# Optimization experiments

Hardware: AMD Instinct MI355X
Metric: run time of the kernel (lower is better)

The kernel has to match this reference:

```python
import jax, jax.numpy as jnp
import numpy as np

PH, PW = 7, 7
SPATIAL_SCALE = 0.0625


def _hat_int(t):
    # Antiderivative of the unit hat (triangle) function phi(t)=max(0,1-|t|),
    # i.e. integral_{-inf}^{t} phi. Piecewise quadratic, saturates to [0,1].
    t = jnp.clip(t, -1.0, 1.0)
    return jnp.where(t <= 0, 0.5 * (t + 1.0) ** 2, 1.0 - 0.5 * (1.0 - t) ** 2)


def _bin_weights(lo, hi, size):
    # lo, hi: [R, P] continuous bin boundaries (in feature-map coordinates).
    # Returns [R, P, size]: exact 1D integral of the hat basis at each integer
    # grid node over [lo, hi]. Bilinear interpolation is the tensor product of
    # 1D hat bases, so the exact 2D PrRoI integral separates into these weights.
    grid = jnp.arange(size, dtype=lo.dtype)
    return _hat_int(hi[..., None] - grid) - _hat_int(lo[..., None] - grid)


def _prroi_pool(features, rois):
    N, C, H, W = features.shape
    R = rois.shape[0]
    dt = features.dtype
    bidx = rois[:, 0].astype(jnp.int32)
    x1 = rois[:, 1] * SPATIAL_SCALE
    y1 = rois[:, 2] * SPATIAL_SCALE
    x2 = rois[:, 3] * SPATIAL_SCALE
    y2 = rois[:, 4] * SPATIAL_SCALE
    roi_w = jnp.maximum(x2 - x1, 0.0)
    roi_h = jnp.maximum(y2 - y1, 0.0)
    bw = roi_w / PW  # [R]
    bh = roi_h / PH
    px = jnp.arange(PW, dtype=dt)
    py = jnp.arange(PH, dtype=dt)
    x_lo = x1[:, None] + px[None, :] * bw[:, None]  # [R, PW]
    x_hi = x_lo + bw[:, None]
    y_lo = y1[:, None] + py[None, :] * bh[:, None]  # [R, PH]
    y_hi = y_lo + bh[:, None]
    Wx = _bin_weights(x_lo, x_hi, W)  # [R, PW, W]
    Wy = _bin_weights(y_lo, y_hi, H)  # [R, PH, H]
    area = bw * bh  # [R]
    inv_area = jnp.where(area > 0, 1.0 / jnp.maximum(area, 1e-12), 0.0)
    out = jnp.zeros((R, C, PH, PW), dtype=dt)
    for n in range(N):  # small fixed batch loop; avoids [R,C,H,W] gather
        m = (bidx == n).astype(dt)
        out = out + jnp.einsum('rph,chw,rqw->rcpq', Wy * m[:, None, None], features[n], Wx)
    return out * inv_area[:, None, None, None]


def setup_inputs() -> dict:
    key = jax.random.key(0)
    k1, k2, k3, k4, k5, k6 = jax.random.split(key, 6)
    N, C, H, W, R = 2, 256, 152, 152, 512
    features = jax.random.normal(k1, (N, C, H, W), dtype=jnp.float32)
    img = H / SPATIAL_SCALE  # 2432 px image
    bidx = jax.random.randint(k2, (R,), 0, N).astype(jnp.float32)
    x1 = jax.random.uniform(k3, (R,), minval=0.0, maxval=img * 0.7)
    y1 = jax.random.uniform(k4, (R,), minval=0.0, maxval=img * 0.7)
    x2 = x1 + jax.random.uniform(k5, (R,), minval=32.0, maxval=img * 0.3)
    y2 = y1 + jax.random.uniform(k6, (R,), minval=32.0, maxval=img * 0.3)
    rois = jnp.stack([bidx, x1, y1, x2, y2], axis=1).astype(jnp.float32)
    return {"features": features, "rois": rois}


def reference(features, rois):
    return _prroi_pool(features, rois)
```

## Files before the change

### kernel.cpp

```cpp
#include <hip/hip_runtime.h>

#define PHH 7
#define PWW 7
static constexpr float SPATIAL_SCALE = 0.0625f;

__device__ __forceinline__ float hat_int(float t) {
    t = fminf(fmaxf(t, -1.0f), 1.0f);
    float a = t + 1.0f, b = 1.0f - t;
    return (t <= 0.0f) ? 0.5f * a * a : 1.0f - 0.5f * b * b;
}

__device__ __forceinline__ float bin_w(float lo, float hi, float g) {
    return hat_int(hi - g) - hat_int(lo - g);
}

__device__ __forceinline__ unsigned short f32_to_bf16_rne(float x) {
    unsigned int u = __float_as_uint(x);
    unsigned int r = 0x7FFFu + ((u >> 16) & 1u);
    return (unsigned short)((u + r) >> 16);
}

__device__ __forceinline__ float bf_lo(unsigned int v) {
    return __uint_as_float(v << 16);
}
__device__ __forceinline__ float bf_hi(unsigned int v) {
    return __uint_as_float(v & 0xFFFF0000u);
}

__global__ __launch_bounds__(256) void transpose_nchw_nhwc_bf16(
    const float* __restrict__ src, unsigned short* __restrict__ dst, int C, int HW)
{
    __shared__ float tile[32][33];
    const int n = blockIdx.z;
    const int hw0 = blockIdx.x * 32;
    const int c0 = blockIdx.y * 32;
    const float* s = src + (size_t)n * C * HW;
    unsigned short* d = dst + (size_t)n * C * HW;
    const int tx = threadIdx.x, ty = threadIdx.y;
    #pragma unroll
    for (int i = ty; i < 32; i += 8) {
        int c = c0 + i, hw = hw0 + tx;
        if (c < C && hw < HW) tile[i][tx] = s[(size_t)c * HW + hw];
    }
    __syncthreads();
    #pragma unroll
    for (int i = ty; i < 32; i += 8) {
        int hw = hw0 + i, c = c0 + tx;
        if (c < C && hw < HW) d[(size_t)hw * C + c] = f32_to_bf16_rne(tile[tx][i]);
    }
}

__global__ __launch_bounds__(256) void prroi_pool_cs2(
    const unsigned short* __restrict__ ft,
    const float* __restrict__ rois,
    float* __restrict__ out,
    int H, int W, int R)
{
    const int nwg = R * PHH;
    int task = (int)blockIdx.x;
    if ((nwg & 7) == 0) {
        const int cpx = nwg >> 3;
        task = (task & 7) * cpx + (task >> 3);
    }
    const int r = task / PHH;
    const int p = task % PHH;

    const int tid = threadIdx.x;
    const int wig = tid >> 6;
    const int lane = tid & 63;
    const int chHalf = wig & 1;
    const int colWave = wig >> 1;
    const int c0 = chHalf * 128 + lane * 2;

    const float* roi = rois + (size_t)r * 5;
    const int b = (int)roi[0];
    const float x1 = roi[1] * SPATIAL_SCALE;
    const float y1 = roi[2] * SPATIAL_SCALE;
    const float x2 = roi[3] * SPATIAL_SCALE;
    const float y2 = roi[4] * SPATIAL_SCALE;
    const float bw = fmaxf(x2 - x1, 0.0f) / (float)PWW;
    const float bh = fmaxf(y2 - y1, 0.0f) / (float)PHH;
    const float area = bw * bh;
    const float inv_area = (area > 0.0f) ? 1.0f / fmaxf(area, 1e-12f) : 0.0f;

    const float ylo = y1 + (float)p * bh;
    const float yhi = ylo + bh;
    const int h0 = max(0, (int)ceilf(ylo - 1.0f));
    const int h1 = min(H - 1, (int)floorf(yhi + 1.0f));
    const int w0 = max(0, (int)ceilf(x1 - 1.0f));
    const int w1 = min(W - 1, (int)floorf(x2 + 1.0f));
    const int nh = min(h1 - h0 + 1, 16);
    const int ww = w1 - w0 + 1;
    const int wwpad = (ww + 7) & ~7;

    __shared__ float wx8[152 * 8];
    __shared__ float wys[16];
    __shared__ float rbuf[2 * 64 * 15];

    for (int i = tid; i < wwpad; i += 256) {
        const float g = (float)(w0 + i);
        #pragma unroll
        for (int q = 0; q < PWW; ++q) {
            const float lo = x1 + (float)q * bw;
            wx8[i * 8 + q] = (i < ww) ? bin_w(lo, lo + bw, g) * inv_area : 0.0f;
        }
        wx8[i * 8 + 7] = 0.0f;
    }
    for (int i = tid; i < nh; i += 256)
        wys[i] = bin_w(ylo, yhi, (float)(h0 + i));
    __syncthreads();

    float acc[PWW][2];
    #pragma unroll
    for (int q = 0; q < PWW; ++q) {
        acc[q][0] = 0.0f;
        acc[q][1] = 0.0f;
    }

    const size_t rowstride = (size_t)W * 256;
    const unsigned short* base =
        ft + ((size_t)b * H + (size_t)h0) * rowstride + (size_t)w0 * 256 + c0;

    for (int chunk = colWave * 8; chunk < ww; chunk += 16) {
        int off[8];
        #pragma unroll
        for (int j = 0; j < 8; ++j)
            off[j] = (chunk + j < ww) ? (chunk + j) * 256 : 0;

        float u[2][8];
        #pragma unroll
        for (int j = 0; j < 8; ++j) { u[0][j] = 0.0f; u[1][j] = 0.0f; }

        auto load_row = [&](unsigned int (&v)[8], int i) {
            const unsigned short* rp = base + (size_t)i * rowstride;
            #pragma unroll
            for (int j = 0; j < 8; ++j)
                v[j] = *(const unsigned int*)(rp + off[j]);
        };
        auto fma_row = [&](const unsigned int (&v)[8], float wy) {
            #pragma unroll
            for (int j = 0; j < 8; ++j) {
                u[0][j] = fmaf(wy, bf_lo(v[j]), u[0][j]);
                u[1][j] = fmaf(wy, bf_hi(v[j]), u[1][j]);
            }
        };

        unsigned int A[8], B[8];
        load_row(A, 0);
        int i = 0;
        while (true) {
            if (i + 1 < nh) load_row(B, i + 1);
            fma_row(A, wys[i]);
            if (++i >= nh) break;
            if (i + 1 < nh) load_row(A, i + 1);
            fma_row(B, wys[i]);
            if (++i >= nh) break;
        }

        #pragma unroll
        for (int j = 0; j < 8; ++j) {
            const float4 wa = *(const float4*)&wx8[(chunk + j) * 8];
            const float4 wb = *(const float4*)&wx8[(chunk + j) * 8 + 4];
            acc[0][0] = fmaf(wa.x, u[0][j], acc[0][0]);
            acc[0][1] = fmaf(wa.x, u[1][j], acc[0][1]);
            acc[1][0] = fmaf(wa.y, u[0][j], acc[1][0]);
            acc[1][1] = fmaf(wa.y, u[1][j], acc[1][1]);
            acc[2][0] = fmaf(wa.z, u[0][j], acc[2][0]);
            acc[2][1] = fmaf(wa.z, u[1][j], acc[2][1]);
            acc[3][0] = fmaf(wa.w, u[0][j], acc[3][0]);
            acc[3][1] = fmaf(wa.w, u[1][j], acc[3][1]);
            acc[4][0] = fmaf(wb.x, u[0][j], acc[4][0]);
            acc[4][1] = fmaf(wb.x, u[1][j], acc[4][1]);
            acc[5][0] = fmaf(wb.y, u[0][j], acc[5][0]);
            acc[5][1] = fmaf(wb.y, u[1][j], acc[5][1]);
            acc[6][0] = fmaf(wb.z, u[0][j], acc[6][0]);
            acc[6][1] = fmaf(wb.z, u[1][j], acc[6][1]);
        }
    }

    float* pbuf = rbuf + chHalf * (64 * 15) + lane * 15;
    if (colWave == 1) {
        #pragma unroll
        for (int q = 0; q < PWW; ++q) {
            pbuf[q * 2 + 0] = acc[q][0];
            pbuf[q * 2 + 1] = acc[q][1];
        }
    }
    __syncthreads();
    if (colWave == 0) {
        float* o = out + ((size_t)r * 256 + c0) * (PHH * PWW) + p * PWW;
        #pragma unroll
        for (int q = 0; q < PWW; ++q) {
            o[q]             = acc[q][0] + pbuf[q * 2 + 0];
            o[PHH * PWW + q] = acc[q][1] + pbuf[q * 2 + 1];
        }
    }
}

__global__ __launch_bounds__(256) void prroi_pool_nchw(
    const float* __restrict__ f, const float* __restrict__ rois,
    float* __restrict__ out, int C, int H, int W, int R)
{
    const int idx = blockIdx.x * blockDim.x + threadIdx.x;
    const int total = R * C * PHH * PWW;
    if (idx >= total) return;
    const int q = idx % PWW;
    const int p = (idx / PWW) % PHH;
    const int c = (idx / (PWW * PHH)) % C;
    const int r = idx / (PWW * PHH * C);
    const float* roi = rois + (size_t)r * 5;
    const int b = (int)roi[0];
    const float x1 = roi[1] * SPATIAL_SCALE;
    const float y1 = roi[2] * SPATIAL_SCALE;
    const float x2 = roi[3] * SPATIAL_SCALE;
    const float y2 = roi[4] * SPATIAL_SCALE;
    const float bw = fmaxf(x2 - x1, 0.0f) / (float)PWW;
    const float bh = fmaxf(y2 - y1, 0.0f) / (float)PHH;
    const float area = bw * bh;
    const float inv_area = (area > 0.0f) ? 1.0f / fmaxf(area, 1e-12f) : 0.0f;
    const float xlo = x1 + (float)q * bw, xhi = xlo + bw;
    const float ylo = y1 + (float)p * bh, yhi = ylo + bh;
    const int h0 = max(0, (int)ceilf(ylo - 1.0f));
    const int h1 = min(H - 1, (int)floorf(yhi + 1.0f));
    const int w0 = max(0, (int)ceilf(xlo - 1.0f));
    const int w1 = min(W - 1, (int)floorf(xhi + 1.0f));
    float acc = 0.0f;
    for (int h = h0; h <= h1; ++h) {
        const float wy = bin_w(ylo, yhi, (float)h);
        const float* fr = f + (((size_t)b * C + c) * H + h) * W;
        for (int w = w0; w <= w1; ++w)
            acc = fmaf(wy * bin_w(xlo, xhi, (float)w), fr[w], acc);
    }
    out[idx] = acc * inv_area;
}

extern "C" void kernel_launch(void* const* d_in, const int* in_sizes, int n_in,
                              void* d_out, int out_size, void* d_ws, size_t ws_size,
                              hipStream_t stream)
{
    const float* features = (const float*)d_in[0];
    const float* rois = (const float*)d_in[1];
    float* out = (float*)d_out;

    const int C = 256, H = 152, W = 152;
    const int N = in_sizes[0] / (C * H * W);
    const int R = in_sizes[1] / 5;

    const size_t need = (size_t)N * C * H * W * sizeof(unsigned short);
    if (ws_size >= need && C == 256) {
        unsigned short* ft = (unsigned short*)d_ws;
        const int HW = H * W;
        dim3 tgrid((HW + 31) / 32, (C + 31) / 32, N);
        transpose_nchw_nhwc_bf16<<<tgrid, dim3(32, 8), 0, stream>>>(features, ft, C, HW);
        prroi_pool_cs2<<<R * PHH, 256, 0, stream>>>(ft, rois, out, H, W, R);
    } else {
        const int total = R * C * PHH * PWW;
        prroi_pool_nchw<<<(total + 255) / 256, 256, 0, stream>>>(features, rois, out, C, H, W, R);
    }
}
```

Measured before the change: 59.01 us.

## Use persistent atomic work-queue pooling kernel and wider bf16 transpose tiles

The pooling kernel becomes persistent: 2048 blocks repeatedly pull (roi, row) tasks from a global atomic counter instead of one block per task. The counter is reset by the transpose kernel that runs first. The transpose now uses 64x64 tiles, converts to bf16 before staging in shared memory, and writes two channels packed into each 32-bit store. The aim is to balance uneven per-task work and cut transpose store traffic. In exchange it drops the XCD-aware task swizzle, adds an atomic and an extra barrier per task, and reserves a fixed workspace offset for the counter.

Result: slower. 94.91 us (+60.9%).

```diff
diff --git a/kernel.cpp b/kernel.cpp
--- a/kernel.cpp
+++ b/kernel.cpp
@@ -27,44 +27,53 @@
     return __uint_as_float(v & 0xFFFF0000u);
 }
 
-__global__ __launch_bounds__(256) void transpose_nchw_nhwc_bf16(
-    const float* __restrict__ src, unsigned short* __restrict__ dst, int C, int HW)
-{
-    __shared__ float tile[32][33];
+__global__ __launch_bounds__(256) void transpose_nchw_nhwc_bf16_v2(
+    const float* __restrict__ src, unsigned short* __restrict__ dst,
+    int C, int HW, int* __restrict__ counter)
+{
+    if (blockIdx.x == 0 && blockIdx.y == 0 && blockIdx.z == 0 && threadIdx.x == 0)
+        *counter = 0;
+
+    __shared__ unsigned short tile[64][66];
     const int n = blockIdx.z;
-    const int hw0 = blockIdx.x * 32;
-    const int c0 = blockIdx.y * 32;
+    const int hw0 = blockIdx.x * 64;
+    const int c0 = blockIdx.y * 64;
     const float* s = src + (size_t)n * C * HW;
     unsigned short* d = dst + (size_t)n * C * HW;
-    const int tx = threadIdx.x, ty = threadIdx.y;
+
+    const int tx = threadIdx.x & 63;
+    const int ty = threadIdx.x >> 6;
     #pragma unroll
-    for (int i = ty; i < 32; i += 8) {
-        int c = c0 + i, hw = hw0 + tx;
-        if (c < C && hw < HW) tile[i][tx] = s[(size_t)c * HW + hw];
+    for (int i = 0; i < 16; ++i) {
+        const int cl = ty * 16 + i;
+        const int c = c0 + cl, hw = hw0 + tx;
+        if (c < C && hw < HW)
+            tile[cl][tx] = f32_to_bf16_rne(s[(size_t)c * HW + hw]);
     }
     __syncthreads();
+
+    const int cl = threadIdx.x & 31;
+    const int hb = threadIdx.x >> 5;
     #pragma unroll
-    for (int i = ty; i < 32; i += 8) {
-        int hw = hw0 + i, c = c0 + tx;
-        if (c < C && hw < HW) d[(size_t)hw * C + c] = f32_to_bf16_rne(tile[tx][i]);
-    }
-}
-
-__global__ __launch_bounds__(256) void prroi_pool_cs2(
+    for (int i = 0; i < 8; ++i) {
+        const int hwl = hb * 8 + i;
+        const int hw = hw0 + hwl;
+        const int c = c0 + 2 * cl;
+        if (hw < HW && c < C) {
+            const unsigned int v = (unsigned int)tile[2 * cl][hwl]
+                                 | ((unsigned int)tile[2 * cl + 1][hwl] << 16);
+            *(unsigned int*)(d + (size_t)hw * C + c) = v;
+        }
+    }
+}
+
+__global__ __launch_bounds__(256) void prroi_pool_persist(
     const unsigned short* __restrict__ ft,
     const float* __restrict__ rois,
     float* __restrict__ out,
-    int H, int W, int R)
-{
-    const int nwg = R * PHH;
-    int task = (int)blockIdx.x;
-    if ((nwg & 7) == 0) {
-        const int cpx = nwg >> 3;
-        task = (task & 7) * cpx + (task >> 3);
-    }
-    const int r = task / PHH;
-    const int p = task % PHH;
-
+    int H, int W, int R, int* __restrict__ counter)
+{
+    const int ntask = R * PHH;
     const int tid = threadIdx.x;
     const int wig = tid >> 6;
     const int lane = tid & 63;
@@ -72,127 +81,134 @@
     const int colWave = wig >> 1;
     const int c0 = chHalf * 128 + lane * 2;
 
-    const float* roi = rois + (size_t)r * 5;
-    const int b = (int)roi[0];
-    const float x1 = roi[1] * SPATIAL_SCALE;
-    const float y1 = roi[2] * SPATIAL_SCALE;
-    const float x2 = roi[3] * SPATIAL_SCALE;
-    const float y2 = roi[4] * SPATIAL_SCALE;
-    const float bw = fmaxf(x2 - x1, 0.0f) / (float)PWW;
-    const float bh = fmaxf(y2 - y1, 0.0f) / (float)PHH;
-    const float area = bw * bh;
-    const float inv_area = (area > 0.0f) ? 1.0f / fmaxf(area, 1e-12f) : 0.0f;
-
-    const float ylo = y1 + (float)p * bh;
-    const float yhi = ylo + bh;
-    const int h0 = max(0, (int)ceilf(ylo - 1.0f));
-    const int h1 = min(H - 1, (int)floorf(yhi + 1.0f));
-    const int w0 = max(0, (int)ceilf(x1 - 1.0f));
-    const int w1 = min(W - 1, (int)floorf(x2 + 1.0f));
-    const int nh = min(h1 - h0 + 1, 16);
-    const int ww = w1 - w0 + 1;
-    const int wwpad = (ww + 7) & ~7;
-
     __shared__ float wx8[152 * 8];
     __shared__ float wys[16];
     __shared__ float rbuf[2 * 64 * 15];
-
-    for (int i = tid; i < wwpad; i += 256) {
-        const float g = (float)(w0 + i);
+    __shared__ int sh_task;
+
+    while (true) {
+        if (tid == 0) sh_task = atomicAdd(counter, 1);
+        __syncthreads();
+        const int task = sh_task;
+        if (task >= ntask) break;
+        const int r = task / PHH;
+        const int p = task % PHH;
+
+        const float* roi = rois + (size_t)r * 5;
+        const int b = (int)roi[0];
+        const float x1 = roi[1] * SPATIAL_SCALE;
+        const float y1 = roi[2] * SPATIAL_SCALE;
+        const float x2 = roi[3] * SPATIAL_SCALE;
+        const float y2 = roi[4] * SPATIAL_SCALE;
+        const float bw = fmaxf(x2 - x1, 0.0f) / (float)PWW;
+        const float bh = fmaxf(y2 - y1, 0.0f) / (float)PHH;
+        const float area = bw * bh;
+        const float inv_area = (area > 0.0f) ? 1.0f / fmaxf(area, 1e-12f) : 0.0f;
+
+        const float ylo = y1 + (float)p * bh;
+        const float yhi = ylo + bh;
+        const int h0 = max(0, (int)ceilf(ylo - 1.0f));
+        const int h1 = min(H - 1, (int)floorf(yhi + 1.0f));
+        const int w0 = max(0, (int)ceilf(x1 - 1.0f));
+        const int w1 = min(W - 1, (int)floorf(x2 + 1.0f));
+        const int nh = min(h1 - h0 + 1, 16);
+        const int ww = w1 - w0 + 1;
+        const int wwpad = (ww + 7) & ~7;
+
+        for (int i = tid; i < wwpad; i += 256) {
+            const float g = (float)(w0 + i);
+            #pragma unroll
+            for (int q = 0; q < PWW; ++q) {
+                const float lo = x1 + (float)q * bw;
+                wx8[i * 8 + q] = (i < ww) ? bin_w(lo, lo + bw, g) * inv_area : 0.0f;
+            }
+            wx8[i * 8 + 7] = 0.0f;
+        }
+        for (int i = tid; i < nh; i += 256)
+            wys[i] = bin_w(ylo, yhi, (float)(h0 + i));
+        __syncthreads();
+
+        float acc[PWW][2];
         #pragma unroll
-        for (int q = 0; q < PWW; ++q) {
-            const float lo = x1 + (float)q * bw;
-            wx8[i * 8 + q] = (i < ww) ? bin_w(lo, lo + bw, g) * inv_area : 0.0f;
-        }
-        wx8[i * 8 + 7] = 0.0f;
-    }
-    for (int i = tid; i < nh; i += 256)
-        wys[i] = bin_w(ylo, yhi, (float)(h0 + i));
-    __syncthreads();
-
-    float acc[PWW][2];
-    #pragma unroll
-    for (int q = 0; q < PWW; ++q) {
-        acc[q][0] = 0.0f;
-        acc[q][1] = 0.0f;
-    }
-
-    const size_t rowstride = (size_t)W * 256;
-    const unsigned short* base =
-        ft + ((size_t)b * H + (size_t)h0) * rowstride + (size_t)w0 * 256 + c0;
-
-    for (int chunk = colWave * 8; chunk < ww; chunk += 16) {
-        int off[8];
-        #pragma unroll
-        for (int j = 0; j < 8; ++j)
-            off[j] = (chunk + j < ww) ? (chunk + j) * 256 : 0;
-
-        float u[2][8];
-        #pragma unroll
-        for (int j = 0; j < 8; ++j) { u[0][j] = 0.0f; u[1][j] = 0.0f; }
-
-        auto load_row = [&](unsigned int (&v)[8], int i) {
-            const unsigned short* rp = base + (size_t)i * rowstride;
+        for (int q = 0; q < PWW; ++q) { acc[q][0] = 0.0f; acc[q][1] = 0.0f; }
+
+        const size_t rowstride = (size_t)W * 256;
+        const unsigned short* base =
+            ft + ((size_t)b * H + (size_t)h0) * rowstride + (size_t)w0 * 256 + c0;
+
+        for (int chunk = colWave * 8; chunk < ww; chunk += 16) {
+            int off[8];
             #pragma unroll
             for (int j = 0; j < 8; ++j)
-                v[j] = *(const unsigned int*)(rp + off[j]);
-        };
-        auto fma_row = [&](const unsigned int (&v)[8], float wy) {
+                off[j] = (chunk + j < ww) ? (chunk + j) * 256 : 0;
+
+            float u[2][8];
+            #pragma unroll
+            for (int j = 0; j < 8; ++j) { u[0][j] = 0.0f; u[1][j] = 0.0f; }
+
+            auto load_row = [&](unsigned int (&v)[8], int i) {
+                const unsigned short* rp = base + (size_t)i * rowstride;
+                #pragma unroll
+                for (int j = 0; j < 8; ++j)
+                    v[j] = *(const unsigned int*)(rp + off[j]);
+            };
+            auto fma_row = [&](const unsigned int (&v)[8], float wy) {
+                #pragma unroll
+                for (int j = 0; j < 8; ++j) {
+                    u[0][j] = fmaf(wy, bf_lo(v[j]), u[0][j]);
+                    u[1][j] = fmaf(wy, bf_hi(v[j]), u[1][j]);
+                }
+            };
+
+            unsigned int A[8], B[8];
+            load_row(A, 0);
+            int i = 0;
+            while (true) {
+                if (i + 1 < nh) load_row(B, i + 1);
+                fma_row(A, wys[i]);
+                if (++i >= nh) break;
+                if (i + 1 < nh) load_row(A, i + 1);
+                fma_row(B, wys[i]);
+                if (++i >= nh) break;
+            }
+
             #pragma unroll
             for (int j = 0; j < 8; ++j) {
-                u[0][j] = fmaf(wy, bf_lo(v[j]), u[0][j]);
-                u[1][j] = fmaf(wy, bf_hi(v[j]), u[1][j]);
-            }
-        };
-
-        unsigned int A[8], B[8];
-        load_row(A, 0);
-        int i = 0;
-        while (true) {
-            if (i + 1 < nh) load_row(B, i + 1);
-            fma_row(A, wys[i]);
-            if (++i >= nh) break;
-            if (i + 1 < nh) load_row(A, i + 1);
-            fma_row(B, wys[i]);
-            if (++i >= nh) break;
-        }
-
-        #pragma unroll
-        for (int j = 0; j < 8; ++j) {
-            const float4 wa = *(const float4*)&wx8[(chunk + j) * 8];
-            const float4 wb = *(const float4*)&wx8[(chunk + j) * 8 + 4];
-            acc[0][0] = fmaf(wa.x, u[0][j], acc[0][0]);
-            acc[0][1] = fmaf(wa.x, u[1][j], acc[0][1]);
-            acc[1][0] = fmaf(wa.y, u[0][j], acc[1][0]);
-            acc[1][1] = fmaf(wa.y, u[1][j], acc[1][1]);
-            acc[2][0] = fmaf(wa.z, u[0][j], acc[2][0]);
-            acc[2][1] = fmaf(wa.z, u[1][j], acc[2][1]);
-            acc[3][0] = fmaf(wa.w, u[0][j], acc[3][0]);
-            acc[3][1] = fmaf(wa.w, u[1][j], acc[3][1]);
-            acc[4][0] = fmaf(wb.x, u[0][j], acc[4][0]);
-            acc[4][1] = fmaf(wb.x, u[1][j], acc[4][1]);
-            acc[5][0] = fmaf(wb.y, u[0][j], acc[5][0]);
-            acc[5][1] = fmaf(wb.y, u[1][j], acc[5][1]);
-            acc[6][0] = fmaf(wb.z, u[0][j], acc[6][0]);
-            acc[6][1] = fmaf(wb.z, u[1][j], acc[6][1]);
-        }
-    }
-
-    float* pbuf = rbuf + chHalf * (64 * 15) + lane * 15;
-    if (colWave == 1) {
-        #pragma unroll
-        for (int q = 0; q < PWW; ++q) {
-            pbuf[q * 2 + 0] = acc[q][0];
-            pbuf[q * 2 + 1] = acc[q][1];
-        }
-    }
-    __syncthreads();
-    if (colWave == 0) {
-        float* o = out + ((size_t)r * 256 + c0) * (PHH * PWW) + p * PWW;
-        #pragma unroll
-        for (int q = 0; q < PWW; ++q) {
-            o[q]             = acc[q][0] + pbuf[q * 2 + 0];
-            o[PHH * PWW + q] = acc[q][1] + pbuf[q * 2 + 1];
+                const float4 wa = *(const float4*)&wx8[(chunk + j) * 8];
+                const float4 wb = *(const float4*)&wx8[(chunk + j) * 8 + 4];
+                acc[0][0] = fmaf(wa.x, u[0][j], acc[0][0]);
+                acc[0][1] = fmaf(wa.x, u[1][j], acc[0][1]);
+                acc[1][0] = fmaf(wa.y, u[0][j], acc[1][0]);
+                acc[1][1] = fmaf(wa.y, u[1][j], acc[1][1]);
+                acc[2][0] = fmaf(wa.z, u[0][j], acc[2][0]);
+                acc[2][1] = fmaf(wa.z, u[1][j], acc[2][1]);
+                acc[3][0] = fmaf(wa.w, u[0][j], acc[3][0]);
+                acc[3][1] = fmaf(wa.w, u[1][j], acc[3][1]);
+                acc[4][0] = fmaf(wb.x, u[0][j], acc[4][0]);
+                acc[4][1] = fmaf(wb.x, u[1][j], acc[4][1]);
+                acc[5][0] = fmaf(wb.y, u[0][j], acc[5][0]);
+                acc[5][1] = fmaf(wb.y, u[1][j], acc[5][1]);
+                acc[6][0] = fmaf(wb.z, u[0][j], acc[6][0]);
+                acc[6][1] = fmaf(wb.z, u[1][j], acc[6][1]);
+            }
+        }
+
+        float* pbuf = rbuf + chHalf * (64 * 15) + lane * 15;
+        if (colWave == 1) {
+            #pragma unroll
+            for (int q = 0; q < PWW; ++q) {
+                pbuf[q * 2 + 0] = acc[q][0];
+                pbuf[q * 2 + 1] = acc[q][1];
+            }
+        }
+        __syncthreads();
+        if (colWave == 0) {
+            float* o = out + ((size_t)r * 256 + c0) * (PHH * PWW) + p * PWW;
+            #pragma unroll
+            for (int q = 0; q < PWW; ++q) {
+                o[q]             = acc[q][0] + pbuf[q * 2 + 0];
+                o[PHH * PWW + q] = acc[q][1] + pbuf[q * 2 + 1];
+            }
         }
     }
 }
@@ -246,13 +262,15 @@
     const int N = in_sizes[0] / (C * H * W);
     const int R = in_sizes[1] / 5;
 
-    const size_t need = (size_t)N * C * H * W * sizeof(unsigned short);
-    if (ws_size >= need && C == 256) {
+    const size_t ft_bytes = (size_t)N * C * H * W * sizeof(unsigned short);
+    const size_t ctr_off = 24u * 1024u * 1024u;
+    if (ws_size >= ctr_off + 64 && ft_bytes <= ctr_off && C == 256) {
         unsigned short* ft = (unsigned short*)d_ws;
+        int* counter = (int*)((char*)d_ws + ctr_off);
         const int HW = H * W;
-        dim3 tgrid((HW + 31) / 32, (C + 31) / 32, N);
-        transpose_nchw_nhwc_bf16<<<tgrid, dim3(32, 8), 0, stream>>>(features, ft, C, HW);
-        prroi_pool_cs2<<<R * PHH, 256, 0, stream>>>(ft, rois, out, H, W, R);
+        dim3 tgrid((HW + 63) / 64, (C + 63) / 64, N);
+        transpose_nchw_nhwc_bf16_v2<<<tgrid, 256, 0, stream>>>(features, ft, C, HW, counter);
+        prroi_pool_persist<<<2048, 256, 0, stream>>>(ft, rois, out, H, W, R, counter);
     } else {
         const int total = R * C * PHH * PWW;
         prroi_pool_nchw<<<(total + 255) / 256, 256, 0, stream>>>(features, rois, out, C, H, W, R);
```
